# Kernel tuning notes

Measured on AMD Instinct MI355X. Metric: run time of the kernel, lower is better.

The kernel has to match this reference:

```python
import jax, jax.numpy as jnp
import numpy as np

B, S, HID, NH = 2, 2048, 1024, 16
HD = HID // NH
NEG = -1e10


def setup_inputs() -> dict:
    key = jax.random.key(0)
    ks = jax.random.split(key, 14)
    s = 0.02
    return {
        "query": jax.random.normal(ks[0], (B, S, HID), jnp.float32),
        "key_": jax.random.normal(ks[1], (B, S, HID), jnp.float32),
        "value": jax.random.normal(ks[2], (B, S, HID), jnp.float32),
        "mask": jax.random.randint(ks[3], (B, 1, 1, S), 0, 2, jnp.int32),
        "Wq": jax.random.normal(ks[4], (HID, HID), jnp.float32) * s,
        "bq": jnp.zeros((HID,), jnp.float32),
        "Wk": jax.random.normal(ks[5], (HID, HID), jnp.float32) * s,
        "bk": jnp.zeros((HID,), jnp.float32),
        "Wv": jax.random.normal(ks[6], (HID, HID), jnp.float32) * s,
        "bv": jnp.zeros((HID,), jnp.float32),
        "Ww": jax.random.normal(ks[7], (HD, HD), jnp.float32) * s,
        "bw": jnp.zeros((HD,), jnp.float32),
        "Wo": jax.random.normal(ks[8], (HID, HID), jnp.float32) * s,
        "bo": jnp.zeros((HID,), jnp.float32),
    }


def reference(query, key_, value, mask, Wq, bq, Wk, bk, Wv, bv, Ww, bw, Wo, bo):
    def heads(x, W, b):
        h = x @ W.T + b                       # [B,S,HID]
        return h.reshape(B, S, NH, HD).transpose(0, 2, 1, 3)  # [B,H,S,D]

    Q = heads(query, Wq, bq)
    K = heads(key_, Wk, bk)
    V = heads(value, Wv, bv)
    # multiplicative: per-head linear on Q before QK^T (no 1/sqrt(d) scale)
    Qw = Q @ Ww.T + bw                        # [B,H,S,D]
    energy = jnp.einsum('bhqd,bhkd->bhqk', Qw, K)
    energy = jnp.where(mask == 0, jnp.float32(NEG), energy)
    attention = jax.nn.softmax(energy, axis=-1)
    x = jnp.einsum('bhqk,bhkd->bhqd', attention, V)  # dropout p=0 (eval)
    x = x.transpose(0, 2, 1, 3).reshape(B, S, HID)
    x = x @ Wo.T + bo
    return (x, attention)
```

## Files before the change

### kernel.cpp

```cpp
#include <hip/hip_runtime.h>
#include <hip/hip_bf16.h>

#define B_    2
#define S_    2048
#define HID_  1024
#define NH_   16
#define HD_   64
#define M_    (B_ * S_)
#define NEGB_ (-1.0e30f)
#define LOG2E 1.44269504088896340736f
#define X_ELEMS 4194304

typedef __bf16 bf16;
typedef bf16  bf16x2 __attribute__((ext_vector_type(2)));
typedef bf16  bf16x4 __attribute__((ext_vector_type(4)));
typedef bf16  bf16x8 __attribute__((ext_vector_type(8)));
typedef float f32x4  __attribute__((ext_vector_type(4)));

static __device__ __forceinline__ f32x4 mfma16(bf16x8 a, bf16x8 b, f32x4 c) {
    return __builtin_amdgcn_mfma_f32_16x16x32_bf16(a, b, c, 0, 0, 0);
}

static __device__ __forceinline__ int pack2(float x, float y) {
    union { bf16x2 h; int i; } u;
    u.h = bf16x2{(bf16)x, (bf16)y};
    return u.i;
}

static __device__ __forceinline__ int swadr(int row, int chunk) {
    return row * 128 + ((chunk ^ (row & 7)) << 4);
}
static __device__ __forceinline__ bf16x8 lds8(const bf16* base, int row, int chunk) {
    return *(const bf16x8*)((const char*)base + swadr(row, chunk));
}


__global__ void cast3(const float* __restrict__ a, const float* __restrict__ b,
                      const float* __restrict__ c, bf16* __restrict__ oa,
                      bf16* __restrict__ ob, bf16* __restrict__ oc) {
    const float* in = blockIdx.y == 0 ? a : blockIdx.y == 1 ? b : c;
    bf16* out = blockIdx.y == 0 ? oa : blockIdx.y == 1 ? ob : oc;
    int i = (blockIdx.x * 256 + threadIdx.x) * 4;
    float4 v = *(const float4*)(in + i);
    out[i + 0] = (bf16)v.x;
    out[i + 1] = (bf16)v.y;
    out[i + 2] = (bf16)v.z;
    out[i + 3] = (bf16)v.w;
}

__global__ __launch_bounds__(256) void fuse_wq(const float* __restrict__ Ww,
                                               const float* __restrict__ Wq,
                                               const float* __restrict__ bq,
                                               const float* __restrict__ bw,
                                               bf16* __restrict__ Wq_eff,
                                               float* __restrict__ bq_eff) {
    __shared__ float ww[64][64];
    const int h = blockIdx.x >> 2, chunk = blockIdx.x & 3;
    const int i = chunk * 256 + threadIdx.x;
    for (int t = threadIdx.x; t < 4096; t += 256) ww[t >> 6][t & 63] = Ww[t];
    __syncthreads();
    float col[64];
    #pragma unroll
    for (int d = 0; d < 64; ++d) col[d] = Wq[(size_t)(h * 64 + d) * 1024 + i];
    for (int j = 0; j < 64; ++j) {
        float acc = 0.f;
        #pragma unroll
        for (int d = 0; d < 64; ++d) acc += ww[j][d] * col[d];
        Wq_eff[(size_t)(h * 64 + j) * 1024 + i] = (bf16)(acc * LOG2E);
    }
    if (chunk == 0 && threadIdx.x < 64) {
        int j = threadIdx.x;
        float acc = bw[j];
        for (int d = 0; d < 64; ++d) acc += ww[j][d] * bq[h * 64 + d];
        bq_eff[h * 64 + j] = acc * LOG2E;
    }
}

__global__ __launch_bounds__(256, 2) void proj3(const float* __restrict__ Aq,
                                                const float* __restrict__ Ak,
                                                const float* __restrict__ Av,
                                                const bf16* __restrict__ W0,
                                                const bf16* __restrict__ W1,
                                                const bf16* __restrict__ W2,
                                                const float* __restrict__ b0,
                                                const float* __restrict__ b1,
                                                const float* __restrict__ b2,
                                                bf16* __restrict__ Qw,
                                                bf16* __restrict__ Kh,
                                                bf16* __restrict__ Vt) {
    __shared__ __align__(16) bf16 Ast[2][128 * 64];
    __shared__ __align__(16) bf16 Wst[2][128 * 64];
    const int z = blockIdx.z;
    const float* A = z == 0 ? Aq : z == 1 ? Ak : Av;
    const bf16* W = z == 0 ? W0 : z == 1 ? W1 : W2;
    const float* bias = z == 0 ? b0 : z == 1 ? b1 : b2;

    const int tid = threadIdx.x;
    const int wave = tid >> 6, lane = tid & 63;
    const int lr = lane & 15, kg = lane >> 4;
    const int mb0 = blockIdx.x * 128;
    const int n0 = blockIdx.y * 128;

    const int arow = tid >> 1, akc = (tid & 1) * 32;
    const int wrow = tid >> 1, wkc = (tid & 1) * 32;

    float4 ar[8];
    bf16x8 wr[4];
    auto loadT = [&](int k0) {
        const float4* ap = (const float4*)(A + (size_t)(mb0 + arow) * HID_ + k0 + akc);
        #pragma unroll
        for (int j = 0; j < 8; ++j) ar[j] = ap[j];
        const bf16* wp = W + (size_t)(n0 + wrow) * HID_ + k0 + wkc;
        #pragma unroll
        for (int j = 0; j < 4; ++j) wr[j] = *(const bf16x8*)(wp + j * 8);
    };
    auto writeT = [&](int buf) {
        #pragma unroll
        for (int c = 0; c < 4; ++c) {
            float4 x0 = ar[2 * c], x1 = ar[2 * c + 1];
            bf16x8 v;
            v[0] = (bf16)x0.x; v[1] = (bf16)x0.y; v[2] = (bf16)x0.z; v[3] = (bf16)x0.w;
            v[4] = (bf16)x1.x; v[5] = (bf16)x1.y; v[6] = (bf16)x1.z; v[7] = (bf16)x1.w;
            *(bf16x8*)((char*)Ast[buf] + swadr(arow, (akc >> 3) + c)) = v;
        }
        #pragma unroll
        for (int c = 0; c < 4; ++c)
            *(bf16x8*)((char*)Wst[buf] + swadr(wrow, (wkc >> 3) + c)) = wr[c];
    };

    f32x4 acc[2][8] = {};
    loadT(0);
    for (int t = 0; t < 16; ++t) {
        const int buf = t & 1;
        writeT(buf);
        if (t < 15) loadT((t + 1) * 64);
        __syncthreads();
        const bf16* ab = Ast[buf];
        const bf16* wb = Wst[buf];
        #pragma unroll
        for (int kp = 0; kp < 2; ++kp) {
            bf16x8 af0 = lds8(ab, wave * 16 + lr, kp * 4 + kg);
            bf16x8 af1 = lds8(ab, 64 + wave * 16 + lr, kp * 4 + kg);
            #pragma unroll
            for (int nf = 0; nf < 8; ++nf) {
                bf16x8 wf = lds8(wb, nf * 16 + lr, kp * 4 + kg);
                acc[0][nf] = mfma16(af0, wf, acc[0][nf]);
                acc[1][nf] = mfma16(af1, wf, acc[1][nf]);
            }
        }
        __syncthreads();
    }

    const int m_base = mb0 + wave * 16;
    #pragma unroll
    for (int t = 0; t < 2; ++t) {
        #pragma unroll
        for (int cg = 0; cg < 8; ++cg) {
            int col = n0 + cg * 16 + lr;
            float bv = bias[col];
            int h = col >> 6, d = col & 63;
            #pragma unroll
            for (int r = 0; r < 4; ++r) {
                int m = m_base + t * 64 + kg * 4 + r;
                int b = m >> 11, s = m & 2047;
                float val = acc[t][cg][r] + bv;
                if (z == 0)
                    Qw[((size_t)(b * NH_ + h) * S_ + s) * HD_ + d] = (bf16)val;
                else if (z == 1)
                    Kh[((size_t)(b * NH_ + h) * S_ + s) * HD_ + d] = (bf16)val;
                else
                    Vt[((size_t)(b * NH_ + h) * HD_ + d) * S_ + s] = (bf16)val;
            }
        }
    }
}

__global__ __launch_bounds__(256, 4) void attn_stats(const bf16* __restrict__ Qw,
                                                     const bf16* __restrict__ Kh,
                                                     const bf16* __restrict__ Vt,
                                                     const int* __restrict__ mask,
                                                     float* __restrict__ lsum_g,
                                                     bf16* __restrict__ Xh) {
    __shared__ __align__(16) float negf[S_];
    __shared__ __align__(16) bf16 Kst[2][4096];
    __shared__ __align__(16) bf16 Vst[2][4096];

    const int tid = threadIdx.x;
    const int lane = tid & 63, wave = tid >> 6;
    const int lr = lane & 15, kg = lane >> 4;

    const int wg = blockIdx.x;
    const int flat = (wg & 7) * 128 + (wg >> 3);
    const int qtile = flat & 31;
    const int bh = flat >> 5;
    const int b = bh >> 4, h = bh & 15;
    const int q0 = qtile * 64 + wave * 16;

    const bf16* Qh = Qw + (size_t)bh * S_ * HD_;
    const bf16* Kb = Kh + (size_t)bh * S_ * HD_;
    const bf16* Vb = Vt + (size_t)bh * HD_ * S_;
    const int*  mb = mask + b * S_;

    for (int t = tid; t < S_; t += 256)
        negf[t] = mb[t] ? 0.f : NEGB_;

    const int srow = tid >> 2;
    const int sc0  = tid & 3;

    bf16x8 a0 = *(const bf16x8*)(Qh + (size_t)(q0 + lr) * HD_ + kg * 8);
    bf16x8 a1 = *(const bf16x8*)(Qh + (size_t)(q0 + lr) * HD_ + 32 + kg * 8);

    const int addrA = (lr + (((kg << 1)    ) & 3) * 16) << 2;
    const int addrB = (lr + (((kg << 1) | 1) & 3) * 16) << 2;
    const bool lt2 = kg < 2;

    __syncthreads();

    bf16x8 kreg[2], vreg[2];
    #pragma unroll
    for (int j = 0; j < 2; ++j) {
        kreg[j] = *(const bf16x8*)(Kb + (size_t)srow * HD_ + (sc0 + 4 * j) * 8);
        vreg[j] = *(const bf16x8*)(Vb + (size_t)srow * S_ + (sc0 + 4 * j) * 8);
    }

    float psum = 0.f;
    f32x4 X[4] = {};
    for (int t = 0; t < 32; ++t) {
        const int buf = t & 1;
        #pragma unroll
        for (int j = 0; j < 2; ++j) {
            *(bf16x8*)((char*)Kst[buf] + swadr(srow, sc0 + 4 * j)) = kreg[j];
            *(bf16x8*)((char*)Vst[buf] + swadr(srow, sc0 + 4 * j)) = vreg[j];
        }
        if (t + 1 < 32) {
            #pragma unroll
            for (int j = 0; j < 2; ++j) {
                kreg[j] = *(const bf16x8*)(Kb + (size_t)((t + 1) * 64 + srow) * HD_ + (sc0 + 4 * j) * 8);
                vreg[j] = *(const bf16x8*)(Vb + (size_t)srow * S_ + (t + 1) * 64 + (sc0 + 4 * j) * 8);
            }
        }
        __syncthreads();
        const bf16* kb = Kst[buf];
        const bf16* vb = Vst[buf];
        #pragma unroll
        for (int s2 = 0; s2 < 2; ++s2) {
            const int rlo = s2 * 32 + lr, rhi = s2 * 32 + 16 + lr;
            bf16x8 k0a = lds8(kb, rlo, kg);
            bf16x8 k1a = lds8(kb, rlo, 4 + kg);
            bf16x8 k0b = lds8(kb, rhi, kg);
            bf16x8 k1b = lds8(kb, rhi, 4 + kg);
            f32x4 e0 = *(const f32x4*)&negf[t * 64 + s2 * 32 + kg * 4];
            f32x4 e1 = *(const f32x4*)&negf[t * 64 + s2 * 32 + 16 + kg * 4];
            e0 = mfma16(k0a, a0, e0);
            e0 = mfma16(k1a, a1, e0);
            e1 = mfma16(k0b, a0, e1);
            e1 = mfma16(k1b, a1, e1);
            f32x4 p0, p1;
            #pragma unroll
            for (int r = 0; r < 4; ++r) { p0[r] = exp2f(e0[r]); p1[r] = exp2f(e1[r]); }
            psum += (p0[0] + p0[1] + p0[2] + p0[3]) + (p1[0] + p1[1] + p1[2] + p1[3]);
            int q0d = pack2(p0[0], p0[1]);
            int q1d = pack2(p0[2], p0[3]);
            int q2d = pack2(p1[0], p1[1]);
            int q3d = pack2(p1[2], p1[3]);
            int bA0 = __builtin_amdgcn_ds_bpermute(addrA, q0d);
            int bA1 = __builtin_amdgcn_ds_bpermute(addrA, q1d);
            int bA2 = __builtin_amdgcn_ds_bpermute(addrA, q2d);
            int bA3 = __builtin_amdgcn_ds_bpermute(addrA, q3d);
            int bB0 = __builtin_amdgcn_ds_bpermute(addrB, q0d);
            int bB1 = __builtin_amdgcn_ds_bpermute(addrB, q1d);
            int bB2 = __builtin_amdgcn_ds_bpermute(addrB, q2d);
            int bB3 = __builtin_amdgcn_ds_bpermute(addrB, q3d);
            union { int d[4]; bf16x8 v; } pau;
            pau.d[0] = lt2 ? bA0 : bA2;
            pau.d[1] = lt2 ? bA1 : bA3;
            pau.d[2] = lt2 ? bB0 : bB2;
            pau.d[3] = lt2 ? bB1 : bB3;
            #pragma unroll
            for (int ds = 0; ds < 4; ++ds) {
                bf16x8 v = lds8(vb, ds * 16 + lr, s2 * 4 + kg);
                X[ds] = mfma16(v, pau.v, X[ds]);
            }
        }
    }

    psum += __shfl_xor(psum, 16);
    psum += __shfl_xor(psum, 32);
    if (lane < 16) lsum_g[(size_t)bh * S_ + q0 + lr] = psum;
    const float linv = 1.0f / psum;

    bf16* xrow = Xh + ((size_t)(b * S_ + q0 + lr)) * HID_ + h * HD_;
    #pragma unroll
    for (int ds = 0; ds < 4; ++ds) {
        bf16x4 xv;
        #pragma unroll
        for (int r = 0; r < 4; ++r) xv[r] = (bf16)(X[ds][r] * linv);
        *(bf16x4*)(xrow + ds * 16 + kg * 4) = xv;
    }
}

__global__ __launch_bounds__(256, 4) void attn_pstream(const bf16* __restrict__ Qw,
                                                       const bf16* __restrict__ Kh,
                                                       const int* __restrict__ mask,
                                                       const float* __restrict__ lsum_g,
                                                       float* __restrict__ attn_out) {
    __shared__ __align__(16) float negf[S_];
    __shared__ __align__(16) bf16 Kst[2][4096];

    const int tid = threadIdx.x;
    const int lane = tid & 63, wave = tid >> 6;
    const int lr = lane & 15, kg = lane >> 4;

    const int wg = blockIdx.x;
    const int flat = (wg & 7) * 128 + (wg >> 3);
    const int qtile = flat & 31;
    const int bh = flat >> 5;
    const int b = bh >> 4;
    const int q0 = qtile * 64 + wave * 16;

    const bf16* Qh = Qw + (size_t)bh * S_ * HD_;
    const bf16* Kb = Kh + (size_t)bh * S_ * HD_;
    const int*  mb = mask + b * S_;
    float* arow = attn_out + (size_t)bh * S_ * S_;

    for (int t = tid; t < S_; t += 256)
        negf[t] = mb[t] ? 0.f : NEGB_;

    const int srow = tid >> 2;
    const int sc0  = tid & 3;

    bf16x8 a0 = *(const bf16x8*)(Qh + (size_t)(q0 + lr) * HD_ + kg * 8);
    bf16x8 a1 = *(const bf16x8*)(Qh + (size_t)(q0 + lr) * HD_ + 32 + kg * 8);
    const float lg2l = __log2f(lsum_g[(size_t)bh * S_ + q0 + lr]);

    __syncthreads();

    bf16x8 kreg[2];
    #pragma unroll
    for (int j = 0; j < 2; ++j)
        kreg[j] = *(const bf16x8*)(Kb + (size_t)srow * HD_ + (sc0 + 4 * j) * 8);

    for (int t = 0; t < 32; ++t) {
        const int buf = t & 1;
        #pragma unroll
        for (int j = 0; j < 2; ++j)
            *(bf16x8*)((char*)Kst[buf] + swadr(srow, sc0 + 4 * j)) = kreg[j];
        if (t + 1 < 32) {
            #pragma unroll
            for (int j = 0; j < 2; ++j)
                kreg[j] = *(const bf16x8*)(Kb + (size_t)((t + 1) * 64 + srow) * HD_ + (sc0 + 4 * j) * 8);
        }
        __syncthreads();
        const bf16* kb = Kst[buf];
        #pragma unroll
        for (int j = 0; j < 4; ++j) {
            const int row = j * 16 + lr;
            bf16x8 k0 = lds8(kb, row, kg);
            bf16x8 k1 = lds8(kb, row, 4 + kg);
            f32x4 nb = *(const f32x4*)&negf[t * 64 + j * 16 + kg * 4];
            f32x4 z;
            #pragma unroll
            for (int r = 0; r < 4; ++r) z[r] = nb[r] - lg2l;
            z = mfma16(k0, a0, z);
            z = mfma16(k1, a1, z);
            f32x4 p;
            #pragma unroll
            for (int r = 0; r < 4; ++r) p[r] = exp2f(z[r]);
            *(f32x4*)(arow + (size_t)(q0 + lr) * S_ + t * 64 + j * 16 + kg * 4) = p;
        }
    }
}

__global__ __launch_bounds__(256, 3) void out_gemm(const bf16* __restrict__ X,
                                                   const bf16* __restrict__ Wo,
                                                   const float* __restrict__ bo,
                                                   float* __restrict__ out) {
    __shared__ __align__(16) bf16 Ast[2][128 * 64];
    __shared__ __align__(16) bf16 Wst[2][64 * 64];

    const int tid = threadIdx.x;
    const int wave = tid >> 6, lane = tid & 63;
    const int lr = lane & 15, kg = lane >> 4;
    const int mb0 = blockIdx.x * 128;
    const int n0 = blockIdx.y * 64;

    const int arow = tid >> 1, akc = (tid & 1) * 32;
    const int wrow = tid >> 2, wkc = (tid & 3) * 16;

    bf16x8 ar[4];
    bf16x8 wr[2];
    auto loadT = [&](int k0) {
        const bf16* ap = X + (size_t)(mb0 + arow) * HID_ + k0 + akc;
        #pragma unroll
        for (int j = 0; j < 4; ++j) ar[j] = *(const bf16x8*)(ap + j * 8);
        const bf16* wp = Wo + (size_t)(n0 + wrow) * HID_ + k0 + wkc;
        wr[0] = *(const bf16x8*)wp;
        wr[1] = *(const bf16x8*)(wp + 8);
    };
    auto writeT = [&](int buf) {
        #pragma unroll
        for (int c = 0; c < 4; ++c)
            *(bf16x8*)((char*)Ast[buf] + swadr(arow, (akc >> 3) + c)) = ar[c];
        *(bf16x8*)((char*)Wst[buf] + swadr(wrow, wkc >> 3)) = wr[0];
        *(bf16x8*)((char*)Wst[buf] + swadr(wrow, (wkc >> 3) + 1)) = wr[1];
    };

    f32x4 acc[2][4] = {};
    loadT(0);
    for (int t = 0; t < 16; ++t) {
        const int buf = t & 1;
        writeT(buf);
        if (t < 15) loadT((t + 1) * 64);
        __syncthreads();
        const bf16* ab = Ast[buf];
        const bf16* wb = Wst[buf];
        #pragma unroll
        for (int kp = 0; kp < 2; ++kp) {
            bf16x8 af0 = lds8(ab, wave * 16 + lr, kp * 4 + kg);
            bf16x8 af1 = lds8(ab, 64 + wave * 16 + lr, kp * 4 + kg);
            #pragma unroll
            for (int nf = 0; nf < 4; ++nf) {
                bf16x8 wf = lds8(wb, nf * 16 + lr, kp * 4 + kg);
                acc[0][nf] = mfma16(af0, wf, acc[0][nf]);
                acc[1][nf] = mfma16(af1, wf, acc[1][nf]);
            }
        }
        __syncthreads();
    }

    const int m_base = mb0 + wave * 16;
    #pragma unroll
    for (int t = 0; t < 2; ++t) {
        #pragma unroll
        for (int cg = 0; cg < 4; ++cg) {
            int col = n0 + cg * 16 + lr;
            float bv = bo[col];
            #pragma unroll
            for (int r = 0; r < 4; ++r)
                out[(size_t)(m_base + t * 64 + kg * 4 + r) * HID_ + col] = acc[t][cg][r] + bv;
        }
    }
}

extern "C" void kernel_launch(void* const* d_in, const int* in_sizes, int n_in,
                              void* d_out, int out_size, void* d_ws, size_t ws_size,
                              hipStream_t stream) {
    const float* query = (const float*)d_in[0];
    const float* key_  = (const float*)d_in[1];
    const float* value = (const float*)d_in[2];
    const int*   mask  = (const int*)d_in[3];
    const float* Wq = (const float*)d_in[4];
    const float* bq = (const float*)d_in[5];
    const float* Wk = (const float*)d_in[6];
    const float* bk = (const float*)d_in[7];
    const float* Wv = (const float*)d_in[8];
    const float* bv = (const float*)d_in[9];
    const float* Ww = (const float*)d_in[10];
    const float* bw = (const float*)d_in[11];
    const float* Wo = (const float*)d_in[12];
    const float* bo = (const float*)d_in[13];
    float* out = (float*)d_out;

    char* ws = (char*)d_ws;
    size_t off = 0;
    auto alloc = [&](size_t bytes) {
        void* p = ws + off;
        off += (bytes + 255) & ~(size_t)255;
        return p;
    };
    bf16*  Wq_eff = (bf16*)alloc((size_t)HID_ * HID_ * 2);
    float* bq_eff = (float*)alloc((size_t)HID_ * 4);
    bf16*  Wk_b   = (bf16*)alloc((size_t)HID_ * HID_ * 2);
    bf16*  Wv_b   = (bf16*)alloc((size_t)HID_ * HID_ * 2);
    bf16*  Wo_b   = (bf16*)alloc((size_t)HID_ * HID_ * 2);
    bf16*  Qw     = (bf16*)alloc((size_t)M_ * HID_ * 2);
    bf16*  Kh     = (bf16*)alloc((size_t)M_ * HID_ * 2);
    bf16*  Vt     = (bf16*)alloc((size_t)M_ * HID_ * 2);
    bf16*  Xh     = (bf16*)alloc((size_t)M_ * HID_ * 2);
    float* lsum_g = (float*)alloc((size_t)B_ * NH_ * S_ * 4);
    (void)ws_size; (void)in_sizes; (void)n_in; (void)out_size;

    dim3 gcast(1024, 3);
    cast3<<<gcast, 256, 0, stream>>>(Wk, Wv, Wo, Wk_b, Wv_b, Wo_b);
    fuse_wq<<<64, 256, 0, stream>>>(Ww, Wq, bq, bw, Wq_eff, bq_eff);

    dim3 gproj(M_ / 128, HID_ / 128, 3);
    proj3<<<gproj, 256, 0, stream>>>(query, key_, value,
                                     Wq_eff, Wk_b, Wv_b,
                                     bq_eff, bk, bv,
                                     Qw, Kh, Vt);

    attn_stats<<<1024, 256, 0, stream>>>(Qw, Kh, Vt, mask, lsum_g, Xh);
    attn_pstream<<<1024, 256, 0, stream>>>(Qw, Kh, mask, lsum_g, out + X_ELEMS);

    dim3 gout(M_ / 128, HID_ / 64);
    out_gemm<<<gout, 256, 0, stream>>>(Xh, Wo_b, bo, out);
}
```

Before: 356.7 us.

## Move PV accumulation into the probability-streaming pass, leaving a sums-only first pass

The first attention pass now only computes softmax row sums. It no longer loads V or runs the PV MFMAs. The second pass computes normalized probabilities once and uses them twice: it writes them to the attention output and, after bf16 packing, accumulates them against V to produce X. The aim is to overlap the PV compute with the store-bound attention write and to drop the separate V traffic and exp work from the first pass. The trade-off is a heavier second kernel with more LDS and register pressure, plus an extra barrier per iteration in the sums pass.

```diff
diff --git a/kernel.cpp b/kernel.cpp
--- a/kernel.cpp
+++ b/kernel.cpp
@@ -175,15 +175,12 @@
     }
 }
 
-__global__ __launch_bounds__(256, 4) void attn_stats(const bf16* __restrict__ Qw,
-                                                     const bf16* __restrict__ Kh,
-                                                     const bf16* __restrict__ Vt,
-                                                     const int* __restrict__ mask,
-                                                     float* __restrict__ lsum_g,
-                                                     bf16* __restrict__ Xh) {
+__global__ __launch_bounds__(256, 4) void attn_sums(const bf16* __restrict__ Qw,
+                                                    const bf16* __restrict__ Kh,
+                                                    const int* __restrict__ mask,
+                                                    float* __restrict__ lsum_g) {
     __shared__ __align__(16) float negf[S_];
     __shared__ __align__(16) bf16 Kst[2][4096];
-    __shared__ __align__(16) bf16 Vst[2][4096];
 
     const int tid = threadIdx.x;
     const int lane = tid & 63, wave = tid >> 6;
@@ -193,12 +190,11 @@
     const int flat = (wg & 7) * 128 + (wg >> 3);
     const int qtile = flat & 31;
     const int bh = flat >> 5;
-    const int b = bh >> 4, h = bh & 15;
+    const int b = bh >> 4;
     const int q0 = qtile * 64 + wave * 16;
 
     const bf16* Qh = Qw + (size_t)bh * S_ * HD_;
     const bf16* Kb = Kh + (size_t)bh * S_ * HD_;
-    const bf16* Vb = Vt + (size_t)bh * HD_ * S_;
     const int*  mb = mask + b * S_;
 
     for (int t = tid; t < S_; t += 256)
@@ -210,38 +206,26 @@
     bf16x8 a0 = *(const bf16x8*)(Qh + (size_t)(q0 + lr) * HD_ + kg * 8);
     bf16x8 a1 = *(const bf16x8*)(Qh + (size_t)(q0 + lr) * HD_ + 32 + kg * 8);
 
-    const int addrA = (lr + (((kg << 1)    ) & 3) * 16) << 2;
-    const int addrB = (lr + (((kg << 1) | 1) & 3) * 16) << 2;
-    const bool lt2 = kg < 2;
-
     __syncthreads();
 
-    bf16x8 kreg[2], vreg[2];
+    bf16x8 kreg[2];
     #pragma unroll
-    for (int j = 0; j < 2; ++j) {
+    for (int j = 0; j < 2; ++j)
         kreg[j] = *(const bf16x8*)(Kb + (size_t)srow * HD_ + (sc0 + 4 * j) * 8);
-        vreg[j] = *(const bf16x8*)(Vb + (size_t)srow * S_ + (sc0 + 4 * j) * 8);
-    }
 
     float psum = 0.f;
-    f32x4 X[4] = {};
     for (int t = 0; t < 32; ++t) {
         const int buf = t & 1;
         #pragma unroll
-        for (int j = 0; j < 2; ++j) {
+        for (int j = 0; j < 2; ++j)
             *(bf16x8*)((char*)Kst[buf] + swadr(srow, sc0 + 4 * j)) = kreg[j];
-            *(bf16x8*)((char*)Vst[buf] + swadr(srow, sc0 + 4 * j)) = vreg[j];
-        }
         if (t + 1 < 32) {
             #pragma unroll
-            for (int j = 0; j < 2; ++j) {
+            for (int j = 0; j < 2; ++j)
                 kreg[j] = *(const bf16x8*)(Kb + (size_t)((t + 1) * 64 + srow) * HD_ + (sc0 + 4 * j) * 8);
-                vreg[j] = *(const bf16x8*)(Vb + (size_t)srow * S_ + (t + 1) * 64 + (sc0 + 4 * j) * 8);
-            }
         }
         __syncthreads();
         const bf16* kb = Kst[buf];
-        const bf16* vb = Vst[buf];
         #pragma unroll
         for (int s2 = 0; s2 < 2; ++s2) {
             const int rlo = s2 * 32 + lr, rhi = s2 * 32 + 16 + lr;
@@ -255,10 +239,108 @@
             e0 = mfma16(k1a, a1, e0);
             e1 = mfma16(k0b, a0, e1);
             e1 = mfma16(k1b, a1, e1);
+            #pragma unroll
+            for (int r = 0; r < 4; ++r)
+                psum += exp2f(e0[r]) + exp2f(e1[r]);
+        }
+        __syncthreads();
+    }
+
+    psum += __shfl_xor(psum, 16);
+    psum += __shfl_xor(psum, 32);
+    if (lane < 16) lsum_g[(size_t)bh * S_ + q0 + lr] = psum;
+}
+
+__global__ __launch_bounds__(256, 4) void attn_main(const bf16* __restrict__ Qw,
+                                                    const bf16* __restrict__ Kh,
+                                                    const bf16* __restrict__ Vt,
+                                                    const int* __restrict__ mask,
+                                                    const float* __restrict__ lsum_g,
+                                                    float* __restrict__ attn_out,
+                                                    bf16* __restrict__ Xh) {
+    __shared__ __align__(16) float negf[S_];
+    __shared__ __align__(16) bf16 Kst[2][4096];
+    __shared__ __align__(16) bf16 Vst[2][4096];
+
+    const int tid = threadIdx.x;
+    const int lane = tid & 63, wave = tid >> 6;
+    const int lr = lane & 15, kg = lane >> 4;
+
+    const int wg = blockIdx.x;
+    const int flat = (wg & 7) * 128 + (wg >> 3);
+    const int qtile = flat & 31;
+    const int bh = flat >> 5;
+    const int b = bh >> 4, h = bh & 15;
+    const int q0 = qtile * 64 + wave * 16;
+
+    const bf16* Qh = Qw + (size_t)bh * S_ * HD_;
+    const bf16* Kb = Kh + (size_t)bh * S_ * HD_;
+    const bf16* Vb = Vt + (size_t)bh * HD_ * S_;
+    const int*  mb = mask + b * S_;
+    float* arow = attn_out + (size_t)bh * S_ * S_;
+
+    for (int t = tid; t < S_; t += 256)
+        negf[t] = mb[t] ? 0.f : NEGB_;
+
+    const int srow = tid >> 2;
+    const int sc0  = tid & 3;
+
+    bf16x8 a0 = *(const bf16x8*)(Qh + (size_t)(q0 + lr) * HD_ + kg * 8);
+    bf16x8 a1 = *(const bf16x8*)(Qh + (size_t)(q0 + lr) * HD_ + 32 + kg * 8);
+    const float lg2l = __log2f(lsum_g[(size_t)bh * S_ + q0 + lr]);
+
+    const int addrA = (lr + (((kg << 1)    ) & 3) * 16) << 2;
+    const int addrB = (lr + (((kg << 1) | 1) & 3) * 16) << 2;
+    const bool lt2 = kg < 2;
+
+    __syncthreads();
+
+    bf16x8 kreg[2], vreg[2];
+    #pragma unroll
+    for (int j = 0; j < 2; ++j) {
+        kreg[j] = *(const bf16x8*)(Kb + (size_t)srow * HD_ + (sc0 + 4 * j) * 8);
+        vreg[j] = *(const bf16x8*)(Vb + (size_t)srow * S_ + (sc0 + 4 * j) * 8);
+    }
+
+    f32x4 X[4] = {};
+    for (int t = 0; t < 32; ++t) {
+        const int buf = t & 1;
+        #pragma unroll
+        for (int j = 0; j < 2; ++j) {
+            *(bf16x8*)((char*)Kst[buf] + swadr(srow, sc0 + 4 * j)) = kreg[j];
+            *(bf16x8*)((char*)Vst[buf] + swadr(srow, sc0 + 4 * j)) = vreg[j];
+        }
+        if (t + 1 < 32) {
+            #pragma unroll
+            for (int j = 0; j < 2; ++j) {
+                kreg[j] = *(const bf16x8*)(Kb + (size_t)((t + 1) * 64 + srow) * HD_ + (sc0 + 4 * j) * 8);
+                vreg[j] = *(const bf16x8*)(Vb + (size_t)srow * S_ + (t + 1) * 64 + (sc0 + 4 * j) * 8);
+            }
+        }
+        __syncthreads();
+        const bf16* kb = Kst[buf];
+        const bf16* vb = Vst[buf];
+        #pragma unroll
+        for (int s2 = 0; s2 < 2; ++s2) {
+            const int rlo = s2 * 32 + lr, rhi = s2 * 32 + 16 + lr;
+            bf16x8 k0a = lds8(kb, rlo, kg);
+            bf16x8 k1a = lds8(kb, rlo, 4 + kg);
+            bf16x8 k0b = lds8(kb, rhi, kg);
+            bf16x8 k1b = lds8(kb, rhi, 4 + kg);
+            f32x4 nb0 = *(const f32x4*)&negf[t * 64 + s2 * 32 + kg * 4];
+            f32x4 nb1 = *(const f32x4*)&negf[t * 64 + s2 * 32 + 16 + kg * 4];
+            f32x4 e0, e1;
+            #pragma unroll
+            for (int r = 0; r < 4; ++r) { e0[r] = nb0[r] - lg2l; e1[r] = nb1[r] - lg2l; }
+            e0 = mfma16(k0a, a0, e0);
+            e0 = mfma16(k1a, a1, e0);
+            e1 = mfma16(k0b, a0, e1);
+            e1 = mfma16(k1b, a1, e1);
             f32x4 p0, p1;
             #pragma unroll
             for (int r = 0; r < 4; ++r) { p0[r] = exp2f(e0[r]); p1[r] = exp2f(e1[r]); }
-            psum += (p0[0] + p0[1] + p0[2] + p0[3]) + (p1[0] + p1[1] + p1[2] + p1[3]);
+            *(f32x4*)(arow + (size_t)(q0 + lr) * S_ + t * 64 + s2 * 32 + kg * 4) = p0;
+            *(f32x4*)(arow + (size_t)(q0 + lr) * S_ + t * 64 + s2 * 32 + 16 + kg * 4) = p1;
             int q0d = pack2(p0[0], p0[1]);
             int q1d = pack2(p0[2], p0[3]);
             int q2d = pack2(p1[0], p1[1]);
@@ -284,90 +366,13 @@
         }
     }
 
-    psum += __shfl_xor(psum, 16);
-    psum += __shfl_xor(psum, 32);
-    if (lane < 16) lsum_g[(size_t)bh * S_ + q0 + lr] = psum;
-    const float linv = 1.0f / psum;
-
     bf16* xrow = Xh + ((size_t)(b * S_ + q0 + lr)) * HID_ + h * HD_;
     #pragma unroll
     for (int ds = 0; ds < 4; ++ds) {
         bf16x4 xv;
         #pragma unroll
-        for (int r = 0; r < 4; ++r) xv[r] = (bf16)(X[ds][r] * linv);
+        for (int r = 0; r < 4; ++r) xv[r] = (bf16)X[ds][r];
         *(bf16x4*)(xrow + ds * 16 + kg * 4) = xv;
-    }
-}
-
-__global__ __launch_bounds__(256, 4) void attn_pstream(const bf16* __restrict__ Qw,
-                                                       const bf16* __restrict__ Kh,
-                                                       const int* __restrict__ mask,
-                                                       const float* __restrict__ lsum_g,
-                                                       float* __restrict__ attn_out) {
-    __shared__ __align__(16) float negf[S_];
-    __shared__ __align__(16) bf16 Kst[2][4096];
-
-    const int tid = threadIdx.x;
-    const int lane = tid & 63, wave = tid >> 6;
-    const int lr = lane & 15, kg = lane >> 4;
-
-    const int wg = blockIdx.x;
-    const int flat = (wg & 7) * 128 + (wg >> 3);
-    const int qtile = flat & 31;
-    const int bh = flat >> 5;
-    const int b = bh >> 4;
-    const int q0 = qtile * 64 + wave * 16;
-
-    const bf16* Qh = Qw + (size_t)bh * S_ * HD_;
-    const bf16* Kb = Kh + (size_t)bh * S_ * HD_;
-    const int*  mb = mask + b * S_;
-    float* arow = attn_out + (size_t)bh * S_ * S_;
-
-    for (int t = tid; t < S_; t += 256)
-        negf[t] = mb[t] ? 0.f : NEGB_;
-
-    const int srow = tid >> 2;
-    const int sc0  = tid & 3;
-
-    bf16x8 a0 = *(const bf16x8*)(Qh + (size_t)(q0 + lr) * HD_ + kg * 8);
-    bf16x8 a1 = *(const bf16x8*)(Qh + (size_t)(q0 + lr) * HD_ + 32 + kg * 8);
-    const float lg2l = __log2f(lsum_g[(size_t)bh * S_ + q0 + lr]);
-
-    __syncthreads();
-
-    bf16x8 kreg[2];
-    #pragma unroll
-    for (int j = 0; j < 2; ++j)
-        kreg[j] = *(const bf16x8*)(Kb + (size_t)srow * HD_ + (sc0 + 4 * j) * 8);
-
-    for (int t = 0; t < 32; ++t) {
-        const int buf = t & 1;
-        #pragma unroll
-        for (int j = 0; j < 2; ++j)
-            *(bf16x8*)((char*)Kst[buf] + swadr(srow, sc0 + 4 * j)) = kreg[j];
-        if (t + 1 < 32) {
-            #pragma unroll
-            for (int j = 0; j < 2; ++j)
-                kreg[j] = *(const bf16x8*)(Kb + (size_t)((t + 1) * 64 + srow) * HD_ + (sc0 + 4 * j) * 8);
-        }
-        __syncthreads();
-        const bf16* kb = Kst[buf];
-        #pragma unroll
-        for (int j = 0; j < 4; ++j) {
-            const int row = j * 16 + lr;
-            bf16x8 k0 = lds8(kb, row, kg);
-            bf16x8 k1 = lds8(kb, row, 4 + kg);
-            f32x4 nb = *(const f32x4*)&negf[t * 64 + j * 16 + kg * 4];
-            f32x4 z;
-            #pragma unroll
-            for (int r = 0; r < 4; ++r) z[r] = nb[r] - lg2l;
-            z = mfma16(k0, a0, z);
-            z = mfma16(k1, a1, z);
-            f32x4 p;
-            #pragma unroll
-            for (int r = 0; r < 4; ++r) p[r] = exp2f(z[r]);
-            *(f32x4*)(arow + (size_t)(q0 + lr) * S_ + t * 64 + j * 16 + kg * 4) = p;
-        }
     }
 }
 
@@ -490,8 +495,8 @@
                                      bq_eff, bk, bv,
                                      Qw, Kh, Vt);
 
-    attn_stats<<<1024, 256, 0, stream>>>(Qw, Kh, Vt, mask, lsum_g, Xh);
-    attn_pstream<<<1024, 256, 0, stream>>>(Qw, Kh, mask, lsum_g, out + X_ELEMS);
+    attn_sums<<<1024, 256, 0, stream>>>(Qw, Kh, mask, lsum_g);
+    attn_main<<<1024, 256, 0, stream>>>(Qw, Kh, Vt, mask, lsum_g, out + X_ELEMS, Xh);
 
     dim3 gout(M_ / 128, HID_ / 64);
     out_gemm<<<gout, 256, 0, stream>>>(Xh, Wo_b, bo, out);
```

Measured after the change: 337.5 us. -5.4%, faster.
